# Kernel optimization log

Measured on AMD Instinct MI355X. Metric: run time of the kernel, lower is better.

## Reference

```python
import jax, jax.numpy as jnp
import numpy as np

D = 1024
H = 16
HD = D // H
L = 2048
B = 1
MLP = 8192
ROPE_BASE = 10000.0
LN_EPS = 1e-5


def layer_norm(x):
    mu = jnp.mean(x, axis=-1, keepdims=True)
    var = jnp.var(x, axis=-1, keepdims=True)
    return (x - mu) / jnp.sqrt(var + LN_EPS)


def rope(x):
    # x: [B, H, L, HD]; non-traditional (rotate-half / NeoX style)
    half = HD // 2
    inv_freq = 1.0 / (ROPE_BASE ** (jnp.arange(0, half, dtype=jnp.float32) / half))
    pos = jnp.arange(x.shape[2], dtype=jnp.float32)
    ang = pos[:, None] * inv_freq[None, :]            # [L, half]
    cos, sin = jnp.cos(ang), jnp.sin(ang)
    x1, x2 = x[..., :half], x[..., half:]
    return jnp.concatenate([x1 * cos - x2 * sin, x2 * cos + x1 * sin], axis=-1).astype(x.dtype)


def setup_inputs() -> dict:
    key = jax.random.key(0)
    ks = jax.random.split(key, 5)
    x = jax.random.normal(ks[0], (B, L, D), dtype=jnp.float32)
    # causal additive mask
    neg = jnp.finfo(jnp.float32).min
    mask = jnp.where(jnp.tril(jnp.ones((L, L), dtype=bool)), 0.0, neg).astype(jnp.float32)
    W_attn = jax.random.normal(ks[1], (3 * D, D), dtype=jnp.float32) * (D ** -0.5)
    W_out = jax.random.normal(ks[2], (D, D), dtype=jnp.float32) * (D ** -0.5)
    W_ffp = jax.random.normal(ks[3], (MLP, D), dtype=jnp.float32) * (D ** -0.5)
    W_ffo = jax.random.normal(ks[4], (D, MLP // 2), dtype=jnp.float32) * ((MLP // 2) ** -0.5)
    return {"x": x, "mask": mask, "W_attn": W_attn, "W_out": W_out, "W_ffp": W_ffp, "W_ffo": W_ffo}


def block(x, mask, W_attn, W_out, W_ffp, W_ffo):
    b, l, d = x.shape
    scale = HD ** -0.5
    # attention branch
    xn = layer_norm(x)
    qkv = xn @ W_attn.T                                    # [B, L, 3D]
    q, k, v = jnp.split(qkv, 3, axis=-1)
    q = q.reshape(b, l, H, HD).transpose(0, 2, 1, 3)       # [B, H, L, HD]
    k = k.reshape(b, l, H, HD).transpose(0, 2, 1, 3)
    v = v.reshape(b, l, H, HD).transpose(0, 2, 1, 3)
    q = rope(q)
    k = rope(k)
    scores = jnp.einsum('bhqd,bhkd->bhqk', q * scale, k)   # [B, H, L, L]
    scores = scores + mask
    probs = jax.nn.softmax(scores.astype(jnp.float32), axis=-1).astype(scores.dtype)
    attn = jnp.einsum('bhqk,bhkd->bhqd', probs, v)
    attn = attn.transpose(0, 2, 1, 3).reshape(b, l, d)
    r = attn @ W_out.T
    h = x + r
    # SwiGLU MLP branch: split ff_proj output, swiglu(x2, x1) = silu(x2) * x1
    g = layer_norm(h) @ W_ffp.T                            # [B, L, MLP]
    x1, x2 = jnp.split(g, 2, axis=-1)
    mlp = (jax.nn.silu(x2) * x1) @ W_ffo.T
    return h + mlp


def reference(x, mask, W_attn, W_out, W_ffp, W_ffo):
    return block(x, mask, W_attn, W_out, W_ffp, W_ffo)
```

## Files before the change

### kernel.cpp

```cpp
#include <hip/hip_runtime.h>
#include <math.h>

#define DMODEL 1024
#define NHEAD  16
#define HDIM   64
#define SEQ    2048
#define MLPD   8192
#define HALF_MLP 4096
static constexpr float LN_EPS_C = 1e-5f;
#define NEG_BIG (-1e30f)
#define SM_SHIFT 16.0f

typedef short bf16x8 __attribute__((ext_vector_type(8)));
typedef float f32x4  __attribute__((ext_vector_type(4)));

__device__ __forceinline__ unsigned short f2b(float f) {
    unsigned int u = __float_as_uint(f);
    u = (u + 0x7FFFu + ((u >> 16) & 1u)) >> 16;
    return (unsigned short)u;
}
__device__ __forceinline__ float b2f(unsigned short h) {
    return __uint_as_float((unsigned int)h << 16);
}

__device__ __forceinline__ void async_copy16(const unsigned short* g, unsigned short* l) {
    __builtin_amdgcn_global_load_lds(
        (const __attribute__((address_space(1))) unsigned int*)(g),
        (__attribute__((address_space(3))) unsigned int*)(l),
        16, 0, 0);
}

__global__ void prep_all(const float* __restrict__ x,
                         const float* __restrict__ W_attn, const float* __restrict__ W_out,
                         const float* __restrict__ W_ffp,  const float* __restrict__ W_ffo,
                         unsigned short* __restrict__ xnb, float2* __restrict__ ct,
                         unsigned short* __restrict__ oa, unsigned short* __restrict__ ob,
                         unsigned short* __restrict__ oc, unsigned short* __restrict__ od) {
    const int bid = blockIdx.x;
    const int tid = threadIdx.x;
    if (bid < SEQ) {
        __shared__ float rs[256], rs2[256];
        float4 v = *(const float4*)(x + (size_t)bid * DMODEL + tid * 4);
        rs[tid]  = v.x + v.y + v.z + v.w;
        rs2[tid] = v.x * v.x + v.y * v.y + v.z * v.z + v.w * v.w;
        __syncthreads();
        for (int off = 128; off > 0; off >>= 1) {
            if (tid < off) { rs[tid] += rs[tid + off]; rs2[tid] += rs2[tid + off]; }
            __syncthreads();
        }
        float mu  = rs[0] * (1.0f / DMODEL);
        float var = rs2[0] * (1.0f / DMODEL) - mu * mu;
        float inv = rsqrtf(var + LN_EPS_C);
        ushort4 o;
        o.x = f2b((v.x - mu) * inv); o.y = f2b((v.y - mu) * inv);
        o.z = f2b((v.z - mu) * inv); o.w = f2b((v.w - mu) * inv);
        *(ushort4*)(xnb + (size_t)bid * DMODEL + tid * 4) = o;
    } else if (bid < SEQ + 256) {
        int idx = (bid - SEQ) * 256 + tid;
        int pos = idx >> 5, p = idx & 31;
        float invf = powf(10000.0f, -(float)p / 32.0f);
        float ang = (float)pos * invf;
        ct[idx] = make_float2(cosf(ang), sinf(ang));
    } else {
        const int n1 = 3 * DMODEL * DMODEL;
        const int n2 = n1 + DMODEL * DMODEL;
        const int n3 = n2 + MLPD * DMODEL;
        int i = ((bid - SEQ - 256) * 256 + tid) * 4;
        const float* src; unsigned short* dst; int off;
        if (i < n1)      { src = W_attn; dst = oa; off = i; }
        else if (i < n2) { src = W_out;  dst = ob; off = i - n1; }
        else if (i < n3) {
            src = W_ffp; off = i - n2;
            int row = off >> 10, col = off & 1023;
            int rp  = (row < HALF_MLP) ? (2 * row) : (2 * (row - HALF_MLP) + 1);
            float4 v = *(const float4*)(src + off);
            ushort4 o;
            o.x = f2b(v.x); o.y = f2b(v.y); o.z = f2b(v.z); o.w = f2b(v.w);
            *(ushort4*)(oc + ((size_t)rp << 10) + col) = o;
            return;
        }
        else             { src = W_ffo; dst = od; off = i - n3; }
        float4 v = *(const float4*)(src + off);
        ushort4 o;
        o.x = f2b(v.x); o.y = f2b(v.y); o.z = f2b(v.z); o.w = f2b(v.w);
        *(ushort4*)(dst + off) = o;
    }
}

__global__ void ln_red2(const float* __restrict__ p0, const float* __restrict__ p1,
                        const float* __restrict__ x, float* __restrict__ h,
                        unsigned short* __restrict__ xnb) {
    const int row = blockIdx.x;
    const int tid = threadIdx.x;
    __shared__ float rs[256], rs2[256];
    const size_t base = (size_t)row * DMODEL + tid * 4;
    float4 a = *(const float4*)(p0 + base);
    float4 b = *(const float4*)(p1 + base);
    float4 r = *(const float4*)(x + base);
    float4 v = { a.x + b.x + r.x, a.y + b.y + r.y, a.z + b.z + r.z, a.w + b.w + r.w };
    *(float4*)(h + base) = v;
    rs[tid]  = v.x + v.y + v.z + v.w;
    rs2[tid] = v.x * v.x + v.y * v.y + v.z * v.z + v.w * v.w;
    __syncthreads();
    for (int off = 128; off > 0; off >>= 1) {
        if (tid < off) { rs[tid] += rs[tid + off]; rs2[tid] += rs2[tid + off]; }
        __syncthreads();
    }
    float mu  = rs[0] * (1.0f / DMODEL);
    float var = rs2[0] * (1.0f / DMODEL) - mu * mu;
    float inv = rsqrtf(var + LN_EPS_C);
    ushort4 o;
    o.x = f2b((v.x - mu) * inv); o.y = f2b((v.y - mu) * inv);
    o.z = f2b((v.z - mu) * inv); o.w = f2b((v.w - mu) * inv);
    *(ushort4*)(xnb + base) = o;
}

__global__ __launch_bounds__(256)
void gemm_qkv(const unsigned short* __restrict__ A, const unsigned short* __restrict__ B,
              const float2* __restrict__ ct,
              unsigned short* __restrict__ Qp, unsigned short* __restrict__ Kp,
              unsigned short* __restrict__ Vt) {
    __shared__ unsigned short As[128 * 32];
    __shared__ unsigned short Bs[128 * 32];
    __shared__ unsigned short St[4][16][72];
    const int tid  = threadIdx.x;
    const int lane = tid & 63;
    const int w    = tid >> 6;
    const int wm   = w >> 1;
    const int wn   = w & 1;
    const int m0   = blockIdx.y * 128;
    const int n0   = blockIdx.x * 128;

    f32x4 acc[4][4] = {};

    const int srow = lane >> 2;
    const int scol = (lane & 3) * 8;
    const unsigned short* Abase = A + (size_t)(m0 + w * 32 + srow) * DMODEL + scol;
    const unsigned short* Bbase = B + (size_t)(n0 + w * 32 + srow) * DMODEL + scol;
    unsigned short* AsW = &As[(w * 32) * 32];
    unsigned short* BsW = &Bs[(w * 32) * 32];

    const int fr = lane & 15;
    const int fk = (lane >> 4) * 8;

    for (int k0 = 0; k0 < DMODEL; k0 += 32) {
        async_copy16(Abase + k0,               AsW);
        async_copy16(Abase + k0 + 16 * DMODEL, AsW + 16 * 32);
        async_copy16(Bbase + k0,               BsW);
        async_copy16(Bbase + k0 + 16 * DMODEL, BsW + 16 * 32);
        __syncthreads();

        bf16x8 af[4], bfr[4];
#pragma unroll
        for (int i = 0; i < 4; ++i)
            af[i] = *(const bf16x8*)(&As[(wm * 64 + i * 16 + fr) * 32 + fk]);
#pragma unroll
        for (int j = 0; j < 4; ++j)
            bfr[j] = *(const bf16x8*)(&Bs[(wn * 64 + j * 16 + fr) * 32 + fk]);
#pragma unroll
        for (int i = 0; i < 4; ++i)
#pragma unroll
            for (int j = 0; j < 4; ++j)
                acc[i][j] = __builtin_amdgcn_mfma_f32_16x16x32_bf16(af[i], bfr[j], acc[i][j], 0, 0, 0);
        __syncthreads();
    }

    const int erow   = (lane >> 4) * 4;
    const int ecol   = lane & 15;
    const int region = blockIdx.x >> 3;
    const int head   = ((n0 + wn * 64) >> 6) & 15;

    if (region == 2) {
        const int sbase = m0 + wm * 64;
        const int dl = lane >> 3;
        const int ch = (lane & 7) * 8;
#pragma unroll
        for (int j = 0; j < 4; ++j) {
#pragma unroll
            for (int i = 0; i < 4; ++i) {
                ushort4 o;
                o.x = f2b(acc[i][j][0]); o.y = f2b(acc[i][j][1]);
                o.z = f2b(acc[i][j][2]); o.w = f2b(acc[i][j][3]);
                *(ushort4*)&St[w][ecol][i * 16 + erow] = o;
            }
#pragma unroll
            for (int p = 0; p < 2; ++p) {
                const int dd = p * 8 + dl;
                bf16x8 v = *(const bf16x8*)&St[w][dd][ch];
                *(bf16x8*)(Vt + ((size_t)head * HDIM + j * 16 + dd) * SEQ + sbase + ch) = v;
            }
        }
    } else {
        unsigned short* P = region ? Kp : Qp;
        const float scale = region ? 1.0f : 0.125f;
        unsigned short* qb = &St[w][erow][0];
#pragma unroll
        for (int i = 0; i < 4; ++i) {
#pragma unroll
            for (int r = 0; r < 4; ++r) {
                const int rowg = m0 + wm * 64 + i * 16 + erow + r;
                const float2* crow = ct + (size_t)rowg * 32;
#pragma unroll
                for (int jj = 0; jj < 2; ++jj) {
                    const float2 cs = crow[jj * 16 + ecol];
                    const float x1 = acc[i][jj][r];
                    const float x2 = acc[i][jj + 2][r];
                    qb[jj * 16 + ecol]      = f2b((x1 * cs.x - x2 * cs.y) * scale);
                    qb[jj * 16 + ecol + 32] = f2b((x2 * cs.x + x1 * cs.y) * scale);
                }
                ushort4 o = *(const ushort4*)&qb[ecol * 4];
                *(ushort4*)(P + ((size_t)head * SEQ + rowg) * HDIM + ecol * 4) = o;
            }
        }
    }
}

__global__ __launch_bounds__(256)
void gemm_mfma_sk(const unsigned short* __restrict__ A, const unsigned short* __restrict__ B,
                  float* __restrict__ P, int Ksub, int lda, int ldb, int ldc) {
    __shared__ unsigned short As[128 * 32];
    __shared__ unsigned short Bs[128 * 32];
    const int tid  = threadIdx.x;
    const int lane = tid & 63;
    const int w    = tid >> 6;
    const int wm   = w >> 1;
    const int wn   = w & 1;
    const int m0   = blockIdx.y * 128;
    const int n0   = blockIdx.x * 128;
    const int kb   = blockIdx.z * Ksub;

    f32x4 acc[4][4] = {};

    const int srow = lane >> 2;
    const int scol = (lane & 3) * 8;
    const unsigned short* Abase = A + (size_t)(m0 + w * 32 + srow) * lda + scol + kb;
    const unsigned short* Bbase = B + (size_t)(n0 + w * 32 + srow) * ldb + scol + kb;
    unsigned short* AsW = &As[(w * 32) * 32];
    unsigned short* BsW = &Bs[(w * 32) * 32];

    const int fr = lane & 15;
    const int fk = (lane >> 4) * 8;

    for (int k0 = 0; k0 < Ksub; k0 += 32) {
        async_copy16(Abase + k0,            AsW);
        async_copy16(Abase + k0 + 16 * lda, AsW + 16 * 32);
        async_copy16(Bbase + k0,            BsW);
        async_copy16(Bbase + k0 + 16 * (size_t)ldb, BsW + 16 * 32);
        __syncthreads();

        bf16x8 af[4], bfr[4];
#pragma unroll
        for (int i = 0; i < 4; ++i)
            af[i] = *(const bf16x8*)(&As[(wm * 64 + i * 16 + fr) * 32 + fk]);
#pragma unroll
        for (int j = 0; j < 4; ++j)
            bfr[j] = *(const bf16x8*)(&Bs[(wn * 64 + j * 16 + fr) * 32 + fk]);
#pragma unroll
        for (int i = 0; i < 4; ++i)
#pragma unroll
            for (int j = 0; j < 4; ++j)
                acc[i][j] = __builtin_amdgcn_mfma_f32_16x16x32_bf16(af[i], bfr[j], acc[i][j], 0, 0, 0);
        __syncthreads();
    }

    float* Pp = P + (size_t)blockIdx.z * SEQ * ldc;
    const int erow = (lane >> 4) * 4;
    const int ecol = lane & 15;
#pragma unroll
    for (int i = 0; i < 4; ++i)
#pragma unroll
        for (int j = 0; j < 4; ++j) {
            const int colg = n0 + wn * 64 + j * 16 + ecol;
#pragma unroll
            for (int r = 0; r < 4; ++r) {
                const int rowg = m0 + wm * 64 + i * 16 + erow + r;
                Pp[(size_t)rowg * ldc + colg] = acc[i][j][r];
            }
        }
}

__global__ void reduce4_kernel(const float* __restrict__ p0, const float* __restrict__ p1,
                               const float* __restrict__ p2, const float* __restrict__ p3,
                               const float* __restrict__ res, float* __restrict__ out) {
    int i = (blockIdx.x * blockDim.x + threadIdx.x) * 4;
    float4 a = *(const float4*)(p0 + i);
    float4 b = *(const float4*)(p1 + i);
    float4 c = *(const float4*)(p2 + i);
    float4 d = *(const float4*)(p3 + i);
    float4 r = *(const float4*)(res + i);
    float4 o = { a.x + b.x + c.x + d.x + r.x, a.y + b.y + c.y + d.y + r.y,
                 a.z + b.z + c.z + d.z + r.z, a.w + b.w + c.w + d.w + r.w };
    *(float4*)(out + i) = o;
}

#define FT  32
#define FNT (DMODEL / FT)
__global__ __launch_bounds__(512, 2)
void gemm_ffp_silu_p(const unsigned short* __restrict__ A,
                     const unsigned short* __restrict__ B,
                     unsigned short* __restrict__ gact) {
    __shared__ __align__(16) unsigned short U[4][2][256 * 32];
    const int tid  = threadIdx.x;
    const int lane = tid & 63;
    const int w    = tid >> 6;
    const int wm   = w >> 2;
    const int wn   = w & 3;
    const int fr   = lane & 15;
    const int quad = lane >> 4;

    const int sid = (blockIdx.x & 7) * 32 + (blockIdx.x >> 3);
    const int tm  = sid & 7;
    const int tn  = sid >> 3;

    const unsigned short* Ag = A + (size_t)(tm * 256) * DMODEL;
    const unsigned short* Bg = B + (size_t)(tn * 256) * DMODEL;

    const int srow = tid >> 2;
    const int scg  = ((tid & 3) ^ ((tid >> 3) & 3)) * 8;
    unsigned short* lba = (unsigned short*)&U[0][0][0] + w * 512;
    unsigned short* lbb = (unsigned short*)&U[0][1][0] + w * 512;

    const int rchunk = (quad ^ ((fr >> 1) & 3)) * 8;

    f32x4 acc[8][4] = {};

#define FFP_STAGE(T)                                                          \
    {                                                                         \
        const int k0_ = (T) * FT;                                             \
        const int sl_ = (T) & 3;                                              \
        const unsigned short* ga_ = Ag + (size_t)srow * DMODEL + k0_ + scg;   \
        const unsigned short* gb_ = Bg + (size_t)srow * DMODEL + k0_ + scg;   \
        unsigned short* la_ = lba + sl_ * 16384;                              \
        unsigned short* lb_ = lbb + sl_ * 16384;                              \
        async_copy16(ga_,                la_);                                \
        async_copy16(ga_ + 128 * DMODEL, la_ + 4096);                         \
        async_copy16(gb_,                lb_);                                \
        async_copy16(gb_ + 128 * DMODEL, lb_ + 4096);                         \
    }

    FFP_STAGE(0)
    FFP_STAGE(1)

    for (int t = 0; t < FNT; ++t) {
        if (t + 2 < FNT) {
            FFP_STAGE(t + 2)
            asm volatile("s_waitcnt vmcnt(8)" ::: "memory");
        } else if (t + 1 < FNT) {
            asm volatile("s_waitcnt vmcnt(4)" ::: "memory");
        } else {
            asm volatile("s_waitcnt vmcnt(0)" ::: "memory");
        }
        __builtin_amdgcn_s_barrier();
        __builtin_amdgcn_sched_barrier(0);

        const unsigned short* As_ = &U[t & 3][0][0];
        const unsigned short* Bs_ = &U[t & 3][1][0];
        bf16x8 af[8], bf[4];
#pragma unroll
        for (int i = 0; i < 8; ++i)
            af[i] = *(const bf16x8*)&As_[(wm * 128 + i * 16 + fr) * 32 + rchunk];
#pragma unroll
        for (int j = 0; j < 4; ++j)
            bf[j] = *(const bf16x8*)&Bs_[(wn * 64 + j * 16 + fr) * 32 + rchunk];

        __builtin_amdgcn_s_setprio(1);
#pragma unroll
        for (int i = 0; i < 8; ++i)
#pragma unroll
            for (int j = 0; j < 4; ++j)
                acc[i][j] = __builtin_amdgcn_mfma_f32_16x16x32_bf16(af[i], bf[j], acc[i][j], 0, 0, 0);
        __builtin_amdgcn_s_setprio(0);
    }
#undef FFP_STAGE

    __syncthreads();
    typedef unsigned short StRow[40];
    StRow* Stw = reinterpret_cast<StRow*>(&U[0][0][0]) + (size_t)w * 128;

    const bool evn = (fr & 1) == 0;
#pragma unroll
    for (int i = 0; i < 8; ++i)
#pragma unroll
        for (int j = 0; j < 4; ++j)
#pragma unroll
            for (int r = 0; r < 4; ++r) {
                float own = acc[i][j][r];
                float oth = __shfl_xor(own, 1);
                if (evn) {
                    float sil = oth / (1.0f + __expf(-oth));
                    Stw[i * 16 + quad * 4 + r][j * 8 + (fr >> 1)] = f2b(sil * own);
                }
            }
    {
        const int growb = tm * 256 + wm * 128;
        const int colb  = tn * 128 + wn * 32;
#pragma unroll
        for (int p = 0; p < 2; ++p) {
            const int rl = p * 64 + lane;
            unsigned short* dst = gact + (size_t)(growb + rl) * HALF_MLP + colb;
            bf16x8 v0 = *(const bf16x8*)&Stw[rl][0];
            bf16x8 v1 = *(const bf16x8*)&Stw[rl][8];
            bf16x8 v2 = *(const bf16x8*)&Stw[rl][16];
            bf16x8 v3 = *(const bf16x8*)&Stw[rl][24];
            *(bf16x8*)(dst + 0)  = v0;
            *(bf16x8*)(dst + 8)  = v1;
            *(bf16x8*)(dst + 16) = v2;
            *(bf16x8*)(dst + 24) = v3;
        }
    }
}

__global__ __launch_bounds__(256)
void fattn_blk(const unsigned short* __restrict__ Qp,
               const unsigned short* __restrict__ Kp,
               const unsigned short* __restrict__ Vt,
               unsigned short* __restrict__ out) {
    __shared__ unsigned short Ks[2][64][64];
    __shared__ unsigned short Vs[2][64][64];
    __shared__ unsigned short Ps[4][16][72];
    const int tid  = threadIdx.x;
    const int lane = tid & 63;
    const int w    = tid >> 6;
    const int fr   = lane & 15;
    const int quad = lane >> 4;

    const int f    = blockIdx.x;
    const int head = ((f & 7) << 1) | ((f >> 3) & 1);
    const int ub   = f >> 4;
    const int qb   = (ub & 1) ? (31 - (ub >> 1)) : (ub >> 1);
    const int m0   = qb * 64 + w * 16;

    const unsigned short* Qg = Qp + (size_t)head * SEQ * HDIM;
    const unsigned short* Kg = Kp + (size_t)head * SEQ * HDIM;
    const unsigned short* Vg = Vt + (size_t)head * HDIM * SEQ;

    const int rA = (w << 3) + (lane >> 3);
    const int cg = ((lane & 7) ^ ((lane >> 3) & 7)) << 3;

    bf16x8 qf[2];
#pragma unroll
    for (int kk = 0; kk < 2; ++kk)
        qf[kk] = *(const bf16x8*)(Qg + (size_t)(m0 + fr) * HDIM + kk * 32 + quad * 8);

    bf16x8 ones;
#pragma unroll
    for (int e = 0; e < 8; ++e) ones[e] = (short)0x3F80;

    f32x4 accO[4] = {};
    f32x4 accL = {};

    const int ntiles = qb + 1;

    {
        const unsigned short* gk = Kg + (size_t)rA * HDIM + cg;
        unsigned short* dk = &Ks[0][w << 3][0];
        async_copy16(gk, dk);
        async_copy16(gk + 32 * HDIM, dk + 32 * 64);
        const unsigned short* gv = Vg + (size_t)rA * SEQ + cg;
        unsigned short* dv = &Vs[0][w << 3][0];
        async_copy16(gv, dv);
        async_copy16(gv + 32 * SEQ, dv + 32 * 64);
    }
    __syncthreads();

    int cur = 0;
    for (int t = 0; t < ntiles; ++t) {
        if (t + 1 < ntiles) {
            const int j1 = (t + 1) * 64;
            const unsigned short* gk = Kg + (size_t)(j1 + rA) * HDIM + cg;
            unsigned short* dk = &Ks[cur ^ 1][w << 3][0];
            async_copy16(gk, dk);
            async_copy16(gk + 32 * HDIM, dk + 32 * 64);
            const unsigned short* gv = Vg + (size_t)rA * SEQ + j1 + cg;
            unsigned short* dv = &Vs[cur ^ 1][w << 3][0];
            async_copy16(gv, dv);
            async_copy16(gv + 32 * SEQ, dv + 32 * 64);
        }

        const int j0 = t * 64;
        f32x4 accS[4] = {};
#pragma unroll
        for (int kk = 0; kk < 2; ++kk) {
#pragma unroll
            for (int j = 0; j < 4; ++j) {
                bf16x8 kf = *(const bf16x8*)
                    &Ks[cur][j * 16 + fr][(((kk << 2) + quad) ^ (fr & 7)) << 3];
                accS[j] = __builtin_amdgcn_mfma_f32_16x16x32_bf16(qf[kk], kf, accS[j], 0, 0, 0);
            }
        }

        if (t == ntiles - 1) {
#pragma unroll
            for (int j = 0; j < 4; ++j)
#pragma unroll
                for (int r = 0; r < 4; ++r)
                    if (j0 + j * 16 + fr > m0 + quad * 4 + r) accS[j][r] = NEG_BIG;
        }

#pragma unroll
        for (int j = 0; j < 4; ++j)
#pragma unroll
            for (int r = 0; r < 4; ++r)
                Ps[w][quad * 4 + r][j * 16 + fr] = f2b(__expf(accS[j][r] - SM_SHIFT));

#pragma unroll
        for (int kk = 0; kk < 2; ++kk) {
            bf16x8 pf = *(const bf16x8*)&Ps[w][fr][kk * 32 + quad * 8];
            accL = __builtin_amdgcn_mfma_f32_16x16x32_bf16(pf, ones, accL, 0, 0, 0);
#pragma unroll
            for (int j = 0; j < 4; ++j) {
                bf16x8 vf = *(const bf16x8*)
                    &Vs[cur][j * 16 + fr][(((kk << 2) + quad) ^ (fr & 7)) << 3];
                accO[j] = __builtin_amdgcn_mfma_f32_16x16x32_bf16(pf, vf, accO[j], 0, 0, 0);
            }
        }

        __syncthreads();
        cur ^= 1;
    }

#pragma unroll
    for (int r = 0; r < 4; ++r) {
        const float inv = 1.0f / accL[r];
        const int qrow = m0 + quad * 4 + r;
#pragma unroll
        for (int j = 0; j < 4; ++j)
            out[(size_t)qrow * DMODEL + head * HDIM + j * 16 + fr] = f2b(accO[j][r] * inv);
    }
}

extern "C" void kernel_launch(void* const* d_in, const int* in_sizes, int n_in,
                              void* d_out, int out_size, void* d_ws, size_t ws_size,
                              hipStream_t stream) {
    const float* x      = (const float*)d_in[0];
    const float* W_attn = (const float*)d_in[2];
    const float* W_out  = (const float*)d_in[3];
    const float* W_ffp  = (const float*)d_in[4];
    const float* W_ffo  = (const float*)d_in[5];
    float* out = (float*)d_out;

    char* wsb = (char*)d_ws;
    unsigned short* wb_attn = (unsigned short*)(wsb);
    unsigned short* wb_out  = (unsigned short*)(wsb + (6u  << 20));
    unsigned short* wb_ffp  = (unsigned short*)(wsb + (8u  << 20));
    unsigned short* wb_ffo  = (unsigned short*)(wsb + (24u << 20));
    float*          h       = (float*)(wsb + (32u << 20));
    unsigned short* xnb     = (unsigned short*)(wsb + (40u << 20));
    unsigned short* attnb   = (unsigned short*)(wsb + (44u << 20));
    unsigned short* gact    = (unsigned short*)(wsb + (48u << 20));
    unsigned short* Qp      = (unsigned short*)(wsb + (64u << 20));
    unsigned short* Kp      = (unsigned short*)(wsb + (68u << 20));
    unsigned short* Vt      = (unsigned short*)(wsb + (72u << 20));
    float*          wout_p  = (float*)(wsb + (76u << 20));
    float2*         ct      = (float2*)(wsb + (92u << 20));
    float*          ffo_p   = (float*)(wsb + (64u << 20));

    {
        int f2b_blocks = (3 * DMODEL * DMODEL + DMODEL * DMODEL + MLPD * DMODEL
                          + DMODEL * HALF_MLP) / 4 / 256;
        prep_all<<<SEQ + 256 + f2b_blocks, 256, 0, stream>>>(
            x, W_attn, W_out, W_ffp, W_ffo, xnb, ct,
            wb_attn, wb_out, wb_ffp, wb_ffo);
    }

    gemm_qkv<<<dim3(3 * DMODEL / 128, SEQ / 128), 256, 0, stream>>>(
        xnb, wb_attn, ct, Qp, Kp, Vt);

    fattn_blk<<<512, 256, 0, stream>>>(Qp, Kp, Vt, attnb);

    gemm_mfma_sk<<<dim3(DMODEL / 128, SEQ / 128, 2), 256, 0, stream>>>(
        attnb, wb_out, wout_p, DMODEL / 2, DMODEL, DMODEL, DMODEL);

    ln_red2<<<SEQ, 256, 0, stream>>>(wout_p, wout_p + (size_t)SEQ * DMODEL, x, h, xnb);

    gemm_ffp_silu_p<<<256, 512, 0, stream>>>(xnb, wb_ffp, gact);

    gemm_mfma_sk<<<dim3(DMODEL / 128, SEQ / 128, 4), 256, 0, stream>>>(
        gact, wb_ffo, ffo_p, HALF_MLP / 4, HALF_MLP, HALF_MLP, DMODEL);

    reduce4_kernel<<<SEQ * DMODEL / 4 / 256, 256, 0, stream>>>(
        ffo_p, ffo_p + (size_t)SEQ * DMODEL, ffo_p + 2 * (size_t)SEQ * DMODEL,
        ffo_p + 3 * (size_t)SEQ * DMODEL, h, out);
}
```

Measured before the change: 297.8 us.

## Split FFP GEMM k-step into two phases interleaving loads with MFMA

Restructures the ff_proj GEMM main loop into two half-iterations. Each half issues part of the next-stage global-to-LDS copies, loads half of the A fragments, and runs half of the MFMAs, with barriers placed between phases. This is a ping-pong style schedule meant to overlap LDS reads and global copies with matrix math and to lower register pressure for the A fragments. It adds more barriers per iteration, and the changed vmcnt accounting could stall or race if the counts are wrong.

```diff
diff --git a/kernel.cpp b/kernel.cpp
--- a/kernel.cpp
+++ b/kernel.cpp
@@ -324,54 +324,78 @@
 
     f32x4 acc[8][4] = {};
 
-#define FFP_STAGE(T)                                                          \
+#define FFP_STAGE_H0(T)                                                       \
     {                                                                         \
         const int k0_ = (T) * FT;                                             \
         const int sl_ = (T) & 3;                                              \
         const unsigned short* ga_ = Ag + (size_t)srow * DMODEL + k0_ + scg;   \
-        const unsigned short* gb_ = Bg + (size_t)srow * DMODEL + k0_ + scg;   \
         unsigned short* la_ = lba + sl_ * 16384;                              \
-        unsigned short* lb_ = lbb + sl_ * 16384;                              \
         async_copy16(ga_,                la_);                                \
         async_copy16(ga_ + 128 * DMODEL, la_ + 4096);                         \
+    }
+#define FFP_STAGE_H1(T)                                                       \
+    {                                                                         \
+        const int k0_ = (T) * FT;                                             \
+        const int sl_ = (T) & 3;                                              \
+        const unsigned short* gb_ = Bg + (size_t)srow * DMODEL + k0_ + scg;   \
+        unsigned short* lb_ = lbb + sl_ * 16384;                              \
         async_copy16(gb_,                lb_);                                \
         async_copy16(gb_ + 128 * DMODEL, lb_ + 4096);                         \
     }
 
-    FFP_STAGE(0)
-    FFP_STAGE(1)
+    FFP_STAGE_H0(0) FFP_STAGE_H1(0)
+    FFP_STAGE_H0(1) FFP_STAGE_H1(1)
+    asm volatile("s_waitcnt vmcnt(4)" ::: "memory");
+    __builtin_amdgcn_s_barrier();
 
     for (int t = 0; t < FNT; ++t) {
-        if (t + 2 < FNT) {
-            FFP_STAGE(t + 2)
-            asm volatile("s_waitcnt vmcnt(8)" ::: "memory");
-        } else if (t + 1 < FNT) {
-            asm volatile("s_waitcnt vmcnt(4)" ::: "memory");
-        } else {
-            asm volatile("s_waitcnt vmcnt(0)" ::: "memory");
-        }
-        __builtin_amdgcn_s_barrier();
-        __builtin_amdgcn_sched_barrier(0);
-
         const unsigned short* As_ = &U[t & 3][0][0];
         const unsigned short* Bs_ = &U[t & 3][1][0];
-        bf16x8 af[8], bf[4];
-#pragma unroll
-        for (int i = 0; i < 8; ++i)
+
+        bf16x8 af[4], bf[4];
+#pragma unroll
+        for (int i = 0; i < 4; ++i)
             af[i] = *(const bf16x8*)&As_[(wm * 128 + i * 16 + fr) * 32 + rchunk];
 #pragma unroll
         for (int j = 0; j < 4; ++j)
             bf[j] = *(const bf16x8*)&Bs_[(wn * 64 + j * 16 + fr) * 32 + rchunk];
-
+        if (t + 2 < FNT) FFP_STAGE_H0(t + 2)
+        __builtin_amdgcn_s_barrier();
+        asm volatile("s_waitcnt lgkmcnt(0)" ::: "memory");
+        __builtin_amdgcn_sched_barrier(0);
         __builtin_amdgcn_s_setprio(1);
 #pragma unroll
-        for (int i = 0; i < 8; ++i)
+        for (int i = 0; i < 4; ++i)
 #pragma unroll
             for (int j = 0; j < 4; ++j)
                 acc[i][j] = __builtin_amdgcn_mfma_f32_16x16x32_bf16(af[i], bf[j], acc[i][j], 0, 0, 0);
         __builtin_amdgcn_s_setprio(0);
-    }
-#undef FFP_STAGE
+        __builtin_amdgcn_s_barrier();
+
+        bf16x8 ag[4];
+#pragma unroll
+        for (int i = 0; i < 4; ++i)
+            ag[i] = *(const bf16x8*)&As_[(wm * 128 + (i + 4) * 16 + fr) * 32 + rchunk];
+        if (t + 2 < FNT) {
+            FFP_STAGE_H1(t + 2)
+            asm volatile("s_waitcnt vmcnt(4)" ::: "memory");
+        } else if (t + 1 < FNT) {
+            asm volatile("s_waitcnt vmcnt(0)" ::: "memory");
+        }
+        __builtin_amdgcn_s_barrier();
+        asm volatile("s_waitcnt lgkmcnt(0)" ::: "memory");
+        __builtin_amdgcn_sched_barrier(0);
+        __builtin_amdgcn_s_setprio(1);
+#pragma unroll
+        for (int i = 0; i < 4; ++i)
+#pragma unroll
+            for (int j = 0; j < 4; ++j)
+                acc[i + 4][j] = __builtin_amdgcn_mfma_f32_16x16x32_bf16(ag[i], bf[j], acc[i + 4][j], 0, 0, 0);
+        __builtin_amdgcn_s_setprio(0);
+        __builtin_amdgcn_s_barrier();
+    }
+#undef FFP_STAGE_H0
+#undef FFP_STAGE_H1
 
     __syncthreads();
     typedef unsigned short StRow[40];
```

Result: no change. 301.3 us (+1.2%).

## Pipeline split-K GEMM with 4-slot async LDS ring and swizzled reads

Applied to the files above, without the earlier changes.

Rewrites the split-K MFMA GEMM main loop to prefetch two stages ahead into a four-slot LDS ring buffer, using explicit vmcnt waits and a single barrier per iteration instead of two __syncthreads. It XOR-swizzles the LDS chunk layout to avoid bank conflicts, raises MFMA wave priority, and sets launch bounds for two blocks per CU. It also adds an initial wait and barrier before the FFP pipeline loop. The larger LDS footprint may limit occupancy, and the single-barrier ring relies on the slot-reuse distance for correctness.

```diff
diff --git a/kernel.cpp b/kernel.cpp
--- a/kernel.cpp
+++ b/kernel.cpp
@@ -215,11 +215,10 @@
     }
 }
 
-__global__ __launch_bounds__(256)
+__global__ __launch_bounds__(256, 2)
 void gemm_mfma_sk(const unsigned short* __restrict__ A, const unsigned short* __restrict__ B,
                   float* __restrict__ P, int Ksub, int lda, int ldb, int ldc) {
-    __shared__ unsigned short As[128 * 32];
-    __shared__ unsigned short Bs[128 * 32];
+    __shared__ __align__(16) unsigned short U[4][2][128 * 32];
     const int tid  = threadIdx.x;
     const int lane = tid & 63;
     const int w    = tid >> 6;
@@ -232,36 +231,62 @@
     f32x4 acc[4][4] = {};
 
     const int srow = lane >> 2;
-    const int scol = (lane & 3) * 8;
-    const unsigned short* Abase = A + (size_t)(m0 + w * 32 + srow) * lda + scol + kb;
-    const unsigned short* Bbase = B + (size_t)(n0 + w * 32 + srow) * ldb + scol + kb;
-    unsigned short* AsW = &As[(w * 32) * 32];
-    unsigned short* BsW = &Bs[(w * 32) * 32];
-
-    const int fr = lane & 15;
-    const int fk = (lane >> 4) * 8;
-
-    for (int k0 = 0; k0 < Ksub; k0 += 32) {
-        async_copy16(Abase + k0,            AsW);
-        async_copy16(Abase + k0 + 16 * lda, AsW + 16 * 32);
-        async_copy16(Bbase + k0,            BsW);
-        async_copy16(Bbase + k0 + 16 * (size_t)ldb, BsW + 16 * 32);
-        __syncthreads();
-
+    const int scg  = ((lane & 3) ^ ((lane >> 3) & 3)) * 8;
+    const int fr   = lane & 15;
+    const int quad = lane >> 4;
+    const int rchunk = (quad ^ ((fr >> 1) & 3)) * 8;
+
+#define SK_STAGE(T)                                                           \
+    {                                                                         \
+        const int kk_ = kb + (T) * 32;                                        \
+        const int sl_ = (T) & 3;                                              \
+        const unsigned short* ga_ = A + (size_t)(m0 + w * 32 + srow) * lda + kk_ + scg; \
+        const unsigned short* gb_ = B + (size_t)(n0 + w * 32 + srow) * ldb + kk_ + scg; \
+        unsigned short* la_ = &U[sl_][0][(w * 32) * 32];                      \
+        unsigned short* lb_ = &U[sl_][1][(w * 32) * 32];                      \
+        async_copy16(ga_,                    la_);                            \
+        async_copy16(ga_ + 16 * (size_t)lda, la_ + 16 * 32);                  \
+        async_copy16(gb_,                    lb_);                            \
+        async_copy16(gb_ + 16 * (size_t)ldb, lb_ + 16 * 32);                  \
+    }
+
+    const int NT = Ksub >> 5;
+    SK_STAGE(0)
+    SK_STAGE(1)
+    asm volatile("s_waitcnt vmcnt(4)" ::: "memory");
+    __builtin_amdgcn_s_barrier();
+
+    for (int t = 0; t < NT; ++t) {
+        if (t + 2 < NT) {
+            SK_STAGE(t + 2)
+            asm volatile("s_waitcnt vmcnt(8)" ::: "memory");
+        } else if (t + 1 < NT) {
+            asm volatile("s_waitcnt vmcnt(4)" ::: "memory");
+        } else {
+            asm volatile("s_waitcnt vmcnt(0)" ::: "memory");
+        }
+        __builtin_amdgcn_s_barrier();
+        __builtin_amdgcn_sched_barrier(0);
+
+        const unsigned short* As_ = &U[t & 3][0][0];
+        const unsigned short* Bs_ = &U[t & 3][1][0];
         bf16x8 af[4], bfr[4];
 #pragma unroll
         for (int i = 0; i < 4; ++i)
-            af[i] = *(const bf16x8*)(&As[(wm * 64 + i * 16 + fr) * 32 + fk]);
+            af[i] = *(const bf16x8*)&As_[(wm * 64 + i * 16 + fr) * 32 + rchunk];
 #pragma unroll
         for (int j = 0; j < 4; ++j)
-            bfr[j] = *(const bf16x8*)(&Bs[(wn * 64 + j * 16 + fr) * 32 + fk]);
+            bfr[j] = *(const bf16x8*)&Bs_[(wn * 64 + j * 16 + fr) * 32 + rchunk];
+
+        __builtin_amdgcn_s_setprio(1);
 #pragma unroll
         for (int i = 0; i < 4; ++i)
 #pragma unroll
             for (int j = 0; j < 4; ++j)
                 acc[i][j] = __builtin_amdgcn_mfma_f32_16x16x32_bf16(af[i], bfr[j], acc[i][j], 0, 0, 0);
-        __syncthreads();
-    }
+        __builtin_amdgcn_s_setprio(0);
+    }
+#undef SK_STAGE
 
     float* Pp = P + (size_t)blockIdx.z * SEQ * ldc;
     const int erow = (lane >> 4) * 4;
@@ -340,6 +365,8 @@
 
     FFP_STAGE(0)
     FFP_STAGE(1)
+    asm volatile("s_waitcnt vmcnt(4)" ::: "memory");
+    __builtin_amdgcn_s_barrier();
 
     for (int t = 0; t < FNT; ++t) {
         if (t + 2 < FNT) {
```

Measured after the change: 289.7 us. 1.03x faster.
